# Optimization experiments

Hardware: AMD Instinct MI355X
Metric: run time of the kernel (lower is better)

The kernel has to match this reference:

```python
import jax, jax.numpy as jnp
import numpy as np

D_FEATURE = 512
D_K = 512
B, LQ, N = 64, 128, 2048
NEG_BIAS = 1e10


def setup_inputs() -> dict:
    key = jax.random.key(0)
    k1, k2, k3, k4, k5, k6 = jax.random.split(key, 6)
    # xavier_uniform bound for Linear(d_feature -> d_k), weight shape [d_k, d_feature]
    bound = float(np.sqrt(6.0 / (D_FEATURE + D_K)))
    metal_feature = jax.random.normal(k1, (B, LQ, D_FEATURE), dtype=jnp.float32)
    x = jax.random.normal(k2, (B, N, D_FEATURE), dtype=jnp.float32)
    mask = jax.random.randint(k3, (B, N), 0, 2, dtype=jnp.int32)
    W_q = jax.random.uniform(k4, (D_K, D_FEATURE), jnp.float32, -bound, bound)
    W_k = jax.random.uniform(k5, (D_K, D_FEATURE), jnp.float32, -bound, bound)
    W_v = jax.random.uniform(k6, (D_K, D_FEATURE), jnp.float32, -bound, bound)
    return {"metal_feature": metal_feature, "x": x, "mask": mask,
            "W_q": W_q, "W_k": W_k, "W_v": W_v}


def reference(metal_feature, x, mask, W_q, W_k, W_v):
    # Q: [B, Lq, d_k], K/V: [B, N, d_k]  (torch Linear: y = x @ W.T, no bias)
    Q = jnp.einsum('blf,kf->blk', metal_feature, W_q)
    K = jnp.einsum('bnf,kf->bnk', x, W_k)
    V = jnp.einsum('bnf,kf->bnk', x, W_v)
    scale = 1.0 / jnp.sqrt(jnp.float32(D_K))
    # scores: [B, Lq, N] with additive mask bias (mask broadcast over queries)
    scores = jnp.einsum('blk,bnk->bln', Q, K) * scale
    scores = scores - (1.0 - mask[:, None, :].astype(scores.dtype)) * NEG_BIAS
    attn = jax.nn.softmax(scores, axis=-1)
    out = jnp.einsum('bln,bnk->blk', attn, V)
    # relu; squeeze(1) is a no-op for Lq>1; dropout identity at eval
    return jax.nn.relu(out)
```

## Files before the change

kernel.cpp:

```cpp
#include <hip/hip_runtime.h>

typedef __attribute__((ext_vector_type(4))) float   f32x4;
typedef __attribute__((ext_vector_type(8))) __bf16  bf16x8;
typedef unsigned short u16;
typedef __attribute__((ext_vector_type(8))) unsigned short u16x8;
typedef __attribute__((ext_vector_type(4))) unsigned short u16x4;

__device__ __forceinline__ u16 f2bf(float f) {
  unsigned u = __builtin_bit_cast(unsigned, f);
  u += 0x7fffu + ((u >> 16) & 1u);
  return (u16)(u >> 16);
}
__device__ __forceinline__ float bf2f(u16 h) {
  unsigned u = ((unsigned)h) << 16;
  return __builtin_bit_cast(float, u);
}

__device__ __forceinline__ void gld16(const void* g, void* l) {
  __builtin_amdgcn_global_load_lds(
      (const __attribute__((address_space(1))) void*)g,
      (__attribute__((address_space(3))) void*)l, 16, 0, 0);
}

template<int AF32, int EPI, int SWZ>
__global__ __launch_bounds__(256)
void gemm_k(const void* __restrict__ Ap, const u16* __restrict__ Bp,
            void* __restrict__ Cp, void* __restrict__ Cp2,
            const int* __restrict__ maskp,
            int K, long sA, long sB, long sC, long sM, int ldc, float scale)
{
  __shared__ float Asf[2][AF32 ? 4096 : 4];
  __shared__ u16   Asb[2][AF32 ? 4 : 4096];
  __shared__ u16   Bs [2][4096];

  int bx = blockIdx.x, by = blockIdx.y;
  if constexpr (SWZ) {
    int nwg = gridDim.x * gridDim.y;
    int h = bx + gridDim.x * by;
    int q = nwg >> 3;
    int s = (h & 7) * q + (h >> 3);
    bx = s % gridDim.x; by = s / gridDim.x;
  }
  const int t = threadIdx.x, z = blockIdx.z;
  const int n0 = bx * 128, m0 = by * 128;
  const int KT = K / 32;
  const u16* Bb = Bp + (long)z * sB;

  const int w = t >> 6, lane = t & 63;
  const int m0w = (w >> 1) * 64, n0w = (w & 1) * 64;
  const int lr = lane & 15, lc = lane >> 4;

  f32x4 acc[4][4];
#pragma unroll
  for (int i = 0; i < 4; i++)
#pragma unroll
    for (int j = 0; j < 4; j++) acc[i][j] = f32x4{0.f, 0.f, 0.f, 0.f};

  auto stage = [&](int buf, int kt) {
    if constexpr (AF32) {
      const float* A = (const float*)Ap + (long)z * sA;
#pragma unroll
      for (int i = 0; i < 4; i++) {
        int chunk = w * 4 + i;
        int row = chunk * 8 + (lane >> 3);
        int cc  = lane & 7;
        const float* g = A + (long)(m0 + row) * K + kt * 32 + ((cc ^ (row & 7)) << 2);
        gld16(g, (void*)&Asf[buf][chunk * 256]);
      }
    } else {
      const u16* A = (const u16*)Ap + (long)z * sA;
#pragma unroll
      for (int i = 0; i < 2; i++) {
        int chunk = w * 2 + i;
        int row = chunk * 16 + (lane >> 2);
        int cc  = lane & 3;
        const u16* g = A + (long)(m0 + row) * K + kt * 32 + ((cc ^ ((row >> 1) & 3)) << 3);
        gld16(g, (void*)&Asb[buf][chunk * 512]);
      }
    }
#pragma unroll
    for (int i = 0; i < 2; i++) {
      int chunk = w * 2 + i;
      int row = chunk * 16 + (lane >> 2);
      int cc  = lane & 3;
      const u16* g = Bb + (long)(n0 + row) * K + kt * 32 + ((cc ^ ((row >> 1) & 3)) << 3);
      gld16(g, (void*)&Bs[buf][chunk * 512]);
    }
  };

  auto compute = [&](int buf) {
    bf16x8 af[4], bv[4];
#pragma unroll
    for (int f = 0; f < 4; f++) {
      const int R = m0w + f * 16 + lr;
      if constexpr (AF32) {
        f32x4 lo = *(const f32x4*)&Asf[buf][R * 32 + (((lc * 2 + 0) ^ (R & 7)) << 2)];
        f32x4 hi = *(const f32x4*)&Asf[buf][R * 32 + (((lc * 2 + 1) ^ (R & 7)) << 2)];
        bf16x8 v;
#pragma unroll
        for (int j = 0; j < 4; j++) { v[j] = (__bf16)lo[j]; v[4 + j] = (__bf16)hi[j]; }
        af[f] = v;
      } else {
        af[f] = __builtin_bit_cast(bf16x8,
            *(const u16x8*)&Asb[buf][R * 32 + ((lc ^ ((R >> 1) & 3)) << 3)]);
      }
      const int R2 = n0w + f * 16 + lr;
      bv[f] = __builtin_bit_cast(bf16x8,
          *(const u16x8*)&Bs[buf][R2 * 32 + ((lc ^ ((R2 >> 1) & 3)) << 3)]);
    }
#pragma unroll
    for (int i = 0; i < 4; i++)
#pragma unroll
      for (int j = 0; j < 4; j++)
        acc[i][j] = __builtin_amdgcn_mfma_f32_16x16x32_bf16(af[i], bv[j], acc[i][j], 0, 0, 0);
  };

  stage(0, 0);
  __syncthreads();
  int cur = 0;
  for (int kt = 1; kt < KT; ++kt) {
    stage(cur ^ 1, kt);
    compute(cur);
    __syncthreads();
    cur ^= 1;
  }
  compute(cur);

#pragma unroll
  for (int i = 0; i < 4; i++) {
#pragma unroll
    for (int j = 0; j < 4; j++) {
      const int mb = m0 + m0w + i * 16 + lc * 4;
      const int n  = n0 + n0w + j * 16 + lr;
      if constexpr (EPI == 0) {
        u16* C = (u16*)Cp + (long)z * sC;
#pragma unroll
        for (int ii = 0; ii < 4; ii++)
          C[(long)(mb + ii) * ldc + n] = f2bf(acc[i][j][ii]);
      } else if constexpr (EPI == 1) {
        if (n < 512) {
          u16* C = (u16*)Cp;
#pragma unroll
          for (int ii = 0; ii < 4; ii++)
            C[(long)(mb + ii) * 512 + n] = f2bf(acc[i][j][ii]);
        } else {
          u16* C2 = (u16*)Cp2;
          const int b = mb >> 11, kv = mb & 2047, d = n - 512;
          u16x4 h;
#pragma unroll
          for (int ii = 0; ii < 4; ii++) h[ii] = f2bf(acc[i][j][ii]);
          *(u16x4*)(C2 + ((long)(b * 512 + d)) * 2048 + kv) = h;
        }
      } else if constexpr (EPI == 2) {
        const int* mk = maskp + (long)z * sM;
        u16* C = (u16*)Cp + (long)z * sC;
        const float bias = mk[n] ? 0.f : -1e10f;
#pragma unroll
        for (int ii = 0; ii < 4; ii++)
          C[(long)(mb + ii) * ldc + n] = f2bf(acc[i][j][ii] * scale + bias);
      } else {
        float* C = (float*)Cp + (long)z * sC;
#pragma unroll
        for (int ii = 0; ii < 4; ii++)
          C[(long)(mb + ii) * ldc + n] = fmaxf(acc[i][j][ii], 0.f);
      }
    }
  }
}

__global__ __launch_bounds__(256)
void wconv_k(const float* __restrict__ Wq, const float* __restrict__ Wk,
             const float* __restrict__ Wv, u16* __restrict__ Wb)
{
  long i4 = (long)blockIdx.x * 256 + threadIdx.x;
  long e  = i4 * 4;
  const float* W = (e < 262144) ? Wq : (e < 524288 ? Wk : Wv);
  long off = e & 262143;
  f32x4 f = *(const f32x4*)(W + off);
  u16x4 h;
#pragma unroll
  for (int j = 0; j < 4; j++) h[j] = f2bf(f[j]);
  *(u16x4*)(Wb + e) = h;
}

__global__ __launch_bounds__(256)
void cvt_k(const float* __restrict__ in, u16* __restrict__ out)
{
  long i = ((long)blockIdx.x * 256 + threadIdx.x) * 8;
  f32x4 a = *(const f32x4*)(in + i);
  f32x4 b = *(const f32x4*)(in + i + 4);
  u16x8 h;
#pragma unroll
  for (int j = 0; j < 4; j++) { h[j] = f2bf(a[j]); h[4 + j] = f2bf(b[j]); }
  *(u16x8*)(out + i) = h;
}

__global__ __launch_bounds__(256)
void softmax_k(u16* __restrict__ S)
{
  const long row = blockIdx.x;
  const int  t   = threadIdx.x;
  u16* R = S + row * 2048;
  u16x8 v = *(const u16x8*)(R + t * 8);
  float f[8];
#pragma unroll
  for (int j = 0; j < 8; j++) f[j] = bf2f(v[j]);
  float m = f[0];
#pragma unroll
  for (int j = 1; j < 8; j++) m = fmaxf(m, f[j]);
#pragma unroll
  for (int off = 32; off > 0; off >>= 1) m = fmaxf(m, __shfl_xor(m, off));
  __shared__ float red[4], red2[4];
  const int w = t >> 6;
  if ((t & 63) == 0) red[w] = m;
  __syncthreads();
  m = fmaxf(fmaxf(red[0], red[1]), fmaxf(red[2], red[3]));
  float e[8], s = 0.f;
#pragma unroll
  for (int j = 0; j < 8; j++) { e[j] = __expf(f[j] - m); s += e[j]; }
#pragma unroll
  for (int off = 32; off > 0; off >>= 1) s += __shfl_xor(s, off);
  if ((t & 63) == 0) red2[w] = s;
  __syncthreads();
  s = red2[0] + red2[1] + red2[2] + red2[3];
  const float inv = 1.f / s;
  u16x8 o;
#pragma unroll
  for (int j = 0; j < 8; j++) o[j] = f2bf(e[j] * inv);
  *(u16x8*)(R + t * 8) = o;
}

extern "C" void kernel_launch(void* const* d_in, const int* in_sizes, int n_in,
                              void* d_out, int out_size, void* d_ws, size_t ws_size,
                              hipStream_t stream)
{
  const float* mf   = (const float*)d_in[0];
  const float* x    = (const float*)d_in[1];
  const int*   mask = (const int*)d_in[2];
  const float* Wq   = (const float*)d_in[3];
  const float* Wk   = (const float*)d_in[4];
  const float* Wv   = (const float*)d_in[5];
  float* out = (float*)d_out;

  u16* ws  = (u16*)d_ws;
  u16* Wb  = ws;
  u16* mfb = Wb + 786432;
  u16* Qb  = mfb + 4194304;
  u16* dyn = Qb + 4194304;

  const size_t fixedB = (size_t)(786432 + 4194304 + 4194304) * 2;
  int CB = 64;
  while (CB > 1 && fixedB + (size_t)CB * 4718592ull > ws_size) CB >>= 1;

  u16* Kc  = dyn;
  u16* Vtc = Kc + (size_t)CB * 1048576;
  u16* Sc  = Vtc + (size_t)CB * 1048576;

  const float scale = 0.044194173824159216f;

  wconv_k<<<768, 256, 0, stream>>>(Wq, Wk, Wv, Wb);
  cvt_k<<<2048, 256, 0, stream>>>(mf, mfb);

  gemm_k<0, 0, 0><<<dim3(4, 64, 1), 256, 0, stream>>>(
      mfb, Wb, Qb, nullptr, nullptr, 512, 0, 0, 0, 0, 512, 1.f);

  for (int bc = 0; bc < 64; bc += CB) {
    const float* xc = x + (long)bc * 2048 * 512;
    gemm_k<1, 1, 1><<<dim3(8, CB * 16, 1), 256, 0, stream>>>(
        xc, Wb + 262144, Kc, Vtc, nullptr, 512, 0, 0, 0, 0, 512, 1.f);
    gemm_k<0, 2, 0><<<dim3(16, 1, CB), 256, 0, stream>>>(
        Qb + (long)bc * 65536, Kc, Sc, nullptr, mask + (long)bc * 2048,
        512, 65536, 1048576, 262144, 2048, 2048, scale);
    softmax_k<<<CB * 128, 256, 0, stream>>>(Sc);
    gemm_k<0, 3, 0><<<dim3(4, 1, CB), 256, 0, stream>>>(
        Sc, Vtc, out + (long)bc * 65536, nullptr, nullptr,
        2048, 262144, 1048576, 65536, 0, 512, 1.f);
  }
}
```

Baseline: 474.4 us.

## Triple-buffer GEMM K-loop with vmcnt waits and stage V-transpose epilogue via LDS

Switches the shared GEMM kernel from double to triple buffering of A/B tiles. Two stages are now in flight, with explicit s_waitcnt vmcnt counts and raw barriers replacing __syncthreads, so global loads overlap more compute. The EPI==1 path writing transposed V now goes through an LDS tile and emits coalesced 16-byte row stores instead of scattered 8-byte stores. This costs 50% more LDS per block, which may lower occupancy, and the hand-tuned vmcnt counts depend on how many loads stage issues.

Result: slower. 499.5 us (+5.3%).

```diff
diff --git a/kernel.cpp b/kernel.cpp
--- a/kernel.cpp
+++ b/kernel.cpp
@@ -29,9 +29,9 @@
             const int* __restrict__ maskp,
             int K, long sA, long sB, long sC, long sM, int ldc, float scale)
 {
-  __shared__ float Asf[2][AF32 ? 4096 : 4];
-  __shared__ u16   Asb[2][AF32 ? 4 : 4096];
-  __shared__ u16   Bs [2][4096];
+  __shared__ float Asf[3][AF32 ? 4096 : 4];
+  __shared__ u16   Asb[3][AF32 ? 4 : 4096];
+  __shared__ u16   Bs [3][4096];
 
   int bx = blockIdx.x, by = blockIdx.y;
   if constexpr (SWZ) {
@@ -115,16 +115,69 @@
         acc[i][j] = __builtin_amdgcn_mfma_f32_16x16x32_bf16(af[i], bv[j], acc[i][j], 0, 0, 0);
   };
 
+#define WAIT_OUT() do { if constexpr (AF32) asm volatile("s_waitcnt vmcnt(6)" ::: "memory"); \
+                        else               asm volatile("s_waitcnt vmcnt(4)" ::: "memory"); } while (0)
+#define WAIT_0()   asm volatile("s_waitcnt vmcnt(0)" ::: "memory")
+#define BAR()      do { __builtin_amdgcn_s_barrier(); __builtin_amdgcn_sched_barrier(0); } while (0)
+
   stage(0, 0);
-  __syncthreads();
-  int cur = 0;
-  for (int kt = 1; kt < KT; ++kt) {
-    stage(cur ^ 1, kt);
-    compute(cur);
-    __syncthreads();
-    cur ^= 1;
-  }
-  compute(cur);
+  stage(1, 1);
+  WAIT_OUT();
+  BAR();
+  for (int kt = 0; kt < KT; ++kt) {
+    if (kt + 2 < KT) stage((kt + 2) % 3, kt + 2);
+    compute(kt % 3);
+    if (kt + 1 < KT) {
+      if (kt + 2 < KT) WAIT_OUT(); else WAIT_0();
+      BAR();
+    }
+  }
+#undef WAIT_OUT
+#undef WAIT_0
+#undef BAR
+
+  if constexpr (EPI == 1) {
+    if (n0 >= 512) {
+      u16* T = (u16*)&Asf[0][0];
+      __syncthreads();
+#pragma unroll
+      for (int i = 0; i < 4; i++)
+#pragma unroll
+        for (int j = 0; j < 4; j++) {
+          const int lkv = m0w + i * 16 + lc * 4;
+          const int ld  = n0w + j * 16 + lr;
+          u16x4 h;
+#pragma unroll
+          for (int ii = 0; ii < 4; ii++) h[ii] = f2bf(acc[i][j][ii]);
+          *(u16x4*)&T[ld * 136 + lkv] = h;
+        }
+      __syncthreads();
+      u16* C2 = (u16*)Cp2;
+      const int b = m0 >> 11;
+      const int kvb = m0 & 2047;
+#pragma unroll
+      for (int p = 0; p < 8; ++p) {
+        const int ld = p * 16 + (t >> 4);
+        const int kq = (t & 15) * 8;
+        u16x8 v = *(const u16x8*)&T[ld * 136 + kq];
+        const long d = (n0 - 512) + ld;
+        *(u16x8*)(C2 + ((long)b * 512 + d) * 2048 + kvb + kq) = v;
+      }
+      return;
+    }
+    u16* C = (u16*)Cp;
+#pragma unroll
+    for (int i = 0; i < 4; i++)
+#pragma unroll
+      for (int j = 0; j < 4; j++) {
+        const int mb = m0 + m0w + i * 16 + lc * 4;
+        const int n  = n0 + n0w + j * 16 + lr;
+#pragma unroll
+        for (int ii = 0; ii < 4; ii++)
+          C[(long)(mb + ii) * 512 + n] = f2bf(acc[i][j][ii]);
+      }
+    return;
+  }
 
 #pragma unroll
   for (int i = 0; i < 4; i++) {
@@ -137,20 +190,6 @@
 #pragma unroll
         for (int ii = 0; ii < 4; ii++)
           C[(long)(mb + ii) * ldc + n] = f2bf(acc[i][j][ii]);
-      } else if constexpr (EPI == 1) {
-        if (n < 512) {
-          u16* C = (u16*)Cp;
-#pragma unroll
-          for (int ii = 0; ii < 4; ii++)
-            C[(long)(mb + ii) * 512 + n] = f2bf(acc[i][j][ii]);
-        } else {
-          u16* C2 = (u16*)Cp2;
-          const int b = mb >> 11, kv = mb & 2047, d = n - 512;
-          u16x4 h;
-#pragma unroll
-          for (int ii = 0; ii < 4; ii++) h[ii] = f2bf(acc[i][j][ii]);
-          *(u16x4*)(C2 + ((long)(b * 512 + d)) * 2048 + kv) = h;
-        }
       } else if constexpr (EPI == 2) {
         const int* mk = maskp + (long)z * sM;
         u16* C = (u16*)Cp + (long)z * sC;
@@ -158,7 +197,7 @@
 #pragma unroll
         for (int ii = 0; ii < 4; ii++)
           C[(long)(mb + ii) * ldc + n] = f2bf(acc[i][j][ii] * scale + bias);
-      } else {
+      } else if constexpr (EPI == 3) {
         float* C = (float*)Cp + (long)z * sC;
 #pragma unroll
         for (int ii = 0; ii < 4; ii++)
```

## Pre-convert x to bf16 and use a 256x256-tile 8-wave pipelined K/V projection kernel

Applied to the files above, without the earlier changes.

Splits the K/V projection into two kernels: a separate pass converts x from fp32 to bf16, and a new kernel computes K and V from the bf16 copy using 256x256 tiles with 512 threads. The new kernel interleaves LDS reads, async global-to-LDS loads and MFMA groups with explicit barriers, waitcnts and priority hints, aiming for more data reuse per tile and better overlap of loads with compute than the old 128x128 fp32-A GEMM. The cost is an extra full read and write of x in bf16 and a larger workspace per batch chunk, which may shrink the chunk size. The old fp32-A path of the generic GEMM kernel is removed.

Result: faster. 403.2 us (-15.0%).

```diff
diff --git a/kernel.cpp b/kernel.cpp
--- a/kernel.cpp
+++ b/kernel.cpp
@@ -15,35 +15,156 @@
   unsigned u = ((unsigned)h) << 16;
   return __builtin_bit_cast(float, u);
 }
-
 __device__ __forceinline__ void gld16(const void* g, void* l) {
   __builtin_amdgcn_global_load_lds(
       (const __attribute__((address_space(1))) void*)g,
       (__attribute__((address_space(3))) void*)l, 16, 0, 0);
 }
 
-template<int AF32, int EPI, int SWZ>
-__global__ __launch_bounds__(256)
-void gemm_k(const void* __restrict__ Ap, const u16* __restrict__ Bp,
-            void* __restrict__ Cp, void* __restrict__ Cp2,
-            const int* __restrict__ maskp,
-            int K, long sA, long sB, long sC, long sM, int ldc, float scale)
-{
-  __shared__ float Asf[2][AF32 ? 4096 : 4];
-  __shared__ u16   Asb[2][AF32 ? 4 : 4096];
-  __shared__ u16   Bs [2][4096];
+
+#define SYNC_MID do { __builtin_amdgcn_sched_barrier(0); __builtin_amdgcn_s_barrier(); \
+  asm volatile("s_waitcnt lgkmcnt(0)" ::: "memory"); __builtin_amdgcn_sched_barrier(0); } while(0)
+#define SYNC_END do { __builtin_amdgcn_sched_barrier(0); __builtin_amdgcn_s_barrier(); \
+  __builtin_amdgcn_sched_barrier(0); } while(0)
+#define VM4 asm volatile("s_waitcnt vmcnt(4)" ::: "memory")
+#define VM0 asm volatile("s_waitcnt vmcnt(0)" ::: "memory")
+
+#define LDA(AQ, S, I0) \
+  _Pragma("unroll") for (int f = 0; f < 2; ++f) \
+  _Pragma("unroll") for (int s = 0; s < 2; ++s) { \
+    const int rl = ((I0)+f)*16 + lr; \
+    AQ[f*2+s] = *(const u16x8*)&SM[((S)*2 + wr)*8192 + rl*64 + (((s*4+lc) ^ (rl&7))*8)]; }
+
+#define LDB(S) \
+  _Pragma("unroll") for (int j = 0; j < 4; ++j) \
+  _Pragma("unroll") for (int s = 0; s < 2; ++s) { \
+    const int rl = (wc&1)*64 + j*16 + lr; \
+    bq[j][s] = *(const u16x8*)&SM[32768 + ((S)*2 + (wc>>1))*8192 + rl*64 + (((s*4+lc) ^ (rl&7))*8)]; }
+
+#define MM(AQ, I0) do { __builtin_amdgcn_s_setprio(1); \
+  _Pragma("unroll") for (int f = 0; f < 2; ++f) \
+  _Pragma("unroll") for (int j = 0; j < 4; ++j) \
+  _Pragma("unroll") for (int s = 0; s < 2; ++s) \
+    acc[(I0)+f][j] = __builtin_amdgcn_mfma_f32_16x16x32_bf16( \
+      __builtin_bit_cast(bf16x8, AQ[f*2+s]), __builtin_bit_cast(bf16x8, bq[j][s]), \
+      acc[(I0)+f][j], 0, 0, 0); \
+  __builtin_amdgcn_s_setprio(0); } while(0)
+
+__global__ __launch_bounds__(512, 1)
+void kv8_k(const u16* __restrict__ xb, const u16* __restrict__ Wkv,
+           u16* __restrict__ Kc, u16* __restrict__ Vt)
+{
+  __shared__ u16 SM[65536];
+  const int t = threadIdx.x;
+  const int w = t >> 6, lane = t & 63;
+  const int wr = w >> 2, wc = w & 3;
+  const int lr = lane & 15, lc = lane >> 4;
 
   int bx = blockIdx.x, by = blockIdx.y;
-  if constexpr (SWZ) {
+  {
     int nwg = gridDim.x * gridDim.y;
-    int h = bx + gridDim.x * by;
+    int h = bx + 4 * by;
     int q = nwg >> 3;
     int s = (h & 7) * q + (h >> 3);
-    bx = s % gridDim.x; by = s / gridDim.x;
-  }
+    bx = s & 3; by = s >> 2;
+  }
+  const int n0 = bx * 256;
+  const int m0 = by * 256;
+  const int KT = 8;
+
+  f32x4 acc[8][4];
+#pragma unroll
+  for (int i = 0; i < 8; i++)
+#pragma unroll
+    for (int j = 0; j < 4; j++) acc[i][j] = f32x4{0.f, 0.f, 0.f, 0.f};
+  u16x8 bq[4][2];
+
+  auto stageA = [&](int T, int h) {
+    const int S = T & 1;
+#pragma unroll
+    for (int r = 0; r < 2; ++r) {
+      const int idx = r * 512 + w * 64;
+      const int row = (idx >> 3) + (lane >> 3);
+      const int slot = lane & 7;
+      const u16* g = xb + (long)(m0 + h * 128 + row) * 512 + T * 64 + ((slot ^ (row & 7)) * 8);
+      gld16(g, (void*)&SM[(S * 2 + h) * 8192 + idx * 8]);
+    }
+  };
+  auto stageB = [&](int T, int h) {
+    const int S = T & 1;
+#pragma unroll
+    for (int r = 0; r < 2; ++r) {
+      const int idx = r * 512 + w * 64;
+      const int row = (idx >> 3) + (lane >> 3);
+      const int slot = lane & 7;
+      const u16* g = Wkv + (long)(n0 + h * 128 + row) * 512 + T * 64 + ((slot ^ (row & 7)) * 8);
+      gld16(g, (void*)&SM[32768 + (S * 2 + h) * 8192 + idx * 8]);
+    }
+  };
+
+  stageA(0, 0); stageA(0, 1);
+  stageB(0, 0); stageB(0, 1);
+  stageB(1, 0); stageB(1, 1);
+  VM4; __builtin_amdgcn_sched_barrier(0);
+  __builtin_amdgcn_s_barrier(); __builtin_amdgcn_sched_barrier(0);
+
+  for (int I = 0; I < KT / 2; ++I) {
+    const int a = 2 * I, b = 2 * I + 1;
+    const bool g2 = (a + 2) < KT;
+    const bool g3 = (b + 2) < KT;
+    { u16x8 aq[4]; LDB(0); LDA(aq, 0, 0); stageA(b, 0);
+      SYNC_MID; MM(aq, 0); SYNC_END; }
+    { u16x8 aq[4]; LDA(aq, 0, 2); stageA(b, 1);
+      SYNC_MID; MM(aq, 2); SYNC_END; }
+    { u16x8 aq[4]; LDA(aq, 0, 4); if (g2) stageB(a + 2, 0);
+      SYNC_MID; MM(aq, 4); SYNC_END; }
+    { u16x8 aq[4]; LDA(aq, 0, 6); if (g2) stageB(a + 2, 1);
+      SYNC_MID; MM(aq, 6); if (g2) { VM4; } else { VM0; } SYNC_END; }
+    { u16x8 aq[4]; LDB(1); LDA(aq, 1, 0); if (g2) stageA(a + 2, 0);
+      SYNC_MID; MM(aq, 0); SYNC_END; }
+    { u16x8 aq[4]; LDA(aq, 1, 2); if (g2) stageA(a + 2, 1);
+      SYNC_MID; MM(aq, 2); SYNC_END; }
+    { u16x8 aq[4]; LDA(aq, 1, 4); if (g3) stageB(b + 2, 0);
+      SYNC_MID; MM(aq, 4); SYNC_END; }
+    { u16x8 aq[4]; LDA(aq, 1, 6); if (g3) stageB(b + 2, 1);
+      SYNC_MID; MM(aq, 6); if (g3) { VM4; } else { VM0; } SYNC_END; }
+  }
+
+#pragma unroll
+  for (int i = 0; i < 8; i++) {
+#pragma unroll
+    for (int j = 0; j < 4; j++) {
+      const int ml = wr * 128 + i * 16 + lc * 4;
+      const int m  = m0 + ml;
+      const int n  = n0 + wc * 64 + j * 16 + lr;
+      if (n0 < 512) {
+#pragma unroll
+        for (int ii = 0; ii < 4; ii++)
+          Kc[(long)(m + ii) * 512 + n] = f2bf(acc[i][j][ii]);
+      } else {
+        const int bb = m >> 11, kv = m & 2047, d = n - 512;
+        u16x4 h;
+#pragma unroll
+        for (int ii = 0; ii < 4; ii++) h[ii] = f2bf(acc[i][j][ii]);
+        *(u16x4*)(Vt + ((long)bb * 512 + d) * 2048 + kv) = h;
+      }
+    }
+  }
+}
+
+template<int EPI>
+__global__ __launch_bounds__(256)
+void gemm_k(const u16* __restrict__ Ap, const u16* __restrict__ Bp,
+            void* __restrict__ Cp, const int* __restrict__ maskp,
+            int K, long sA, long sB, long sC, long sM, int ldc, float scale)
+{
+  __shared__ u16 Asb[2][4096];
+  __shared__ u16 Bs [2][4096];
+
   const int t = threadIdx.x, z = blockIdx.z;
-  const int n0 = bx * 128, m0 = by * 128;
+  const int n0 = blockIdx.x * 128, m0 = blockIdx.y * 128;
   const int KT = K / 32;
+  const u16* Ab = Ap + (long)z * sA;
   const u16* Bb = Bp + (long)z * sB;
 
   const int w = t >> 6, lane = t & 63;
@@ -57,53 +178,26 @@
     for (int j = 0; j < 4; j++) acc[i][j] = f32x4{0.f, 0.f, 0.f, 0.f};
 
   auto stage = [&](int buf, int kt) {
-    if constexpr (AF32) {
-      const float* A = (const float*)Ap + (long)z * sA;
-#pragma unroll
-      for (int i = 0; i < 4; i++) {
-        int chunk = w * 4 + i;
-        int row = chunk * 8 + (lane >> 3);
-        int cc  = lane & 7;
-        const float* g = A + (long)(m0 + row) * K + kt * 32 + ((cc ^ (row & 7)) << 2);
-        gld16(g, (void*)&Asf[buf][chunk * 256]);
-      }
-    } else {
-      const u16* A = (const u16*)Ap + (long)z * sA;
-#pragma unroll
-      for (int i = 0; i < 2; i++) {
-        int chunk = w * 2 + i;
-        int row = chunk * 16 + (lane >> 2);
-        int cc  = lane & 3;
-        const u16* g = A + (long)(m0 + row) * K + kt * 32 + ((cc ^ ((row >> 1) & 3)) << 3);
-        gld16(g, (void*)&Asb[buf][chunk * 512]);
-      }
-    }
 #pragma unroll
     for (int i = 0; i < 2; i++) {
-      int chunk = w * 2 + i;
-      int row = chunk * 16 + (lane >> 2);
-      int cc  = lane & 3;
+      int chunk = w * 2 + i, row = chunk * 16 + (lane >> 2), cc = lane & 3;
+      const u16* g = Ab + (long)(m0 + row) * K + kt * 32 + ((cc ^ ((row >> 1) & 3)) << 3);
+      gld16(g, (void*)&Asb[buf][chunk * 512]);
+    }
+#pragma unroll
+    for (int i = 0; i < 2; i++) {
+      int chunk = w * 2 + i, row = chunk * 16 + (lane >> 2), cc = lane & 3;
       const u16* g = Bb + (long)(n0 + row) * K + kt * 32 + ((cc ^ ((row >> 1) & 3)) << 3);
       gld16(g, (void*)&Bs[buf][chunk * 512]);
     }
   };
-
   auto compute = [&](int buf) {
     bf16x8 af[4], bv[4];
 #pragma unroll
     for (int f = 0; f < 4; f++) {
       const int R = m0w + f * 16 + lr;
-      if constexpr (AF32) {
-        f32x4 lo = *(const f32x4*)&Asf[buf][R * 32 + (((lc * 2 + 0) ^ (R & 7)) << 2)];
-        f32x4 hi = *(const f32x4*)&Asf[buf][R * 32 + (((lc * 2 + 1) ^ (R & 7)) << 2)];
-        bf16x8 v;
-#pragma unroll
-        for (int j = 0; j < 4; j++) { v[j] = (__bf16)lo[j]; v[4 + j] = (__bf16)hi[j]; }
-        af[f] = v;
-      } else {
-        af[f] = __builtin_bit_cast(bf16x8,
-            *(const u16x8*)&Asb[buf][R * 32 + ((lc ^ ((R >> 1) & 3)) << 3)]);
-      }
+      af[f] = __builtin_bit_cast(bf16x8,
+          *(const u16x8*)&Asb[buf][R * 32 + ((lc ^ ((R >> 1) & 3)) << 3)]);
       const int R2 = n0w + f * 16 + lr;
       bv[f] = __builtin_bit_cast(bf16x8,
           *(const u16x8*)&Bs[buf][R2 * 32 + ((lc ^ ((R2 >> 1) & 3)) << 3)]);
@@ -137,20 +231,6 @@
 #pragma unroll
         for (int ii = 0; ii < 4; ii++)
           C[(long)(mb + ii) * ldc + n] = f2bf(acc[i][j][ii]);
-      } else if constexpr (EPI == 1) {
-        if (n < 512) {
-          u16* C = (u16*)Cp;
-#pragma unroll
-          for (int ii = 0; ii < 4; ii++)
-            C[(long)(mb + ii) * 512 + n] = f2bf(acc[i][j][ii]);
-        } else {
-          u16* C2 = (u16*)Cp2;
-          const int b = mb >> 11, kv = mb & 2047, d = n - 512;
-          u16x4 h;
-#pragma unroll
-          for (int ii = 0; ii < 4; ii++) h[ii] = f2bf(acc[i][j][ii]);
-          *(u16x4*)(C2 + ((long)(b * 512 + d)) * 2048 + kv) = h;
-        }
       } else if constexpr (EPI == 2) {
         const int* mk = maskp + (long)z * sM;
         u16* C = (u16*)Cp + (long)z * sC;
@@ -250,10 +330,11 @@
 
   const size_t fixedB = (size_t)(786432 + 4194304 + 4194304) * 2;
   int CB = 64;
-  while (CB > 1 && fixedB + (size_t)CB * 4718592ull > ws_size) CB >>= 1;
-
-  u16* Kc  = dyn;
-  u16* Vtc = Kc + (size_t)CB * 1048576;
+  while (CB > 1 && fixedB + (size_t)CB * 6815744ull > ws_size) CB >>= 1;
+
+  u16* xbc = dyn;
+  u16* Kc  = xbc + (size_t)CB * 1048576;
+  u16* Vtc = Kc  + (size_t)CB * 1048576;
   u16* Sc  = Vtc + (size_t)CB * 1048576;
 
   const float scale = 0.044194173824159216f;
@@ -261,19 +342,19 @@
   wconv_k<<<768, 256, 0, stream>>>(Wq, Wk, Wv, Wb);
   cvt_k<<<2048, 256, 0, stream>>>(mf, mfb);
 
-  gemm_k<0, 0, 0><<<dim3(4, 64, 1), 256, 0, stream>>>(
-      mfb, Wb, Qb, nullptr, nullptr, 512, 0, 0, 0, 0, 512, 1.f);
+  gemm_k<0><<<dim3(4, 64, 1), 256, 0, stream>>>(
+      mfb, Wb, Qb, nullptr, 512, 0, 0, 0, 0, 512, 1.f);
 
   for (int bc = 0; bc < 64; bc += CB) {
     const float* xc = x + (long)bc * 2048 * 512;
-    gemm_k<1, 1, 1><<<dim3(8, CB * 16, 1), 256, 0, stream>>>(
-        xc, Wb + 262144, Kc, Vtc, nullptr, 512, 0, 0, 0, 0, 512, 1.f);
-    gemm_k<0, 2, 0><<<dim3(16, 1, CB), 256, 0, stream>>>(
-        Qb + (long)bc * 65536, Kc, Sc, nullptr, mask + (long)bc * 2048,
+    cvt_k<<<CB * 512, 256, 0, stream>>>(xc, xbc);
+    kv8_k<<<dim3(4, CB * 8, 1), 512, 0, stream>>>(xbc, Wb + 262144, Kc, Vtc);
+    gemm_k<2><<<dim3(16, 1, CB), 256, 0, stream>>>(
+        Qb + (long)bc * 65536, Kc, Sc, mask + (long)bc * 2048,
         512, 65536, 1048576, 262144, 2048, 2048, scale);
     softmax_k<<<CB * 128, 256, 0, stream>>>(Sc);
-    gemm_k<0, 3, 0><<<dim3(4, 1, CB), 256, 0, stream>>>(
-        Sc, Vtc, out + (long)bc * 65536, nullptr, nullptr,
+    gemm_k<3><<<dim3(4, 1, CB), 256, 0, stream>>>(
+        Sc, Vtc, out + (long)bc * 65536, nullptr,
         2048, 262144, 1048576, 65536, 0, 512, 1.f);
   }
 }
```
